# Kernel tuning notes

Measured on AMD Instinct MI355X. Metric: run time of the kernel, lower is better.

The kernel has to match this reference:

```python
import jax, jax.numpy as jnp
import numpy as np

G = 1.0 / 7.0  # grid cell size


def _iou(a, b):
    # a, b: tuples (x1, y1, x2, y2) of broadcastable arrays
    ix1 = jnp.maximum(a[0], b[0])
    iy1 = jnp.maximum(a[1], b[1])
    ix2 = jnp.minimum(a[2], b[2])
    iy2 = jnp.minimum(a[3], b[3])
    inter = jnp.clip(ix2 - ix1, 0.0) * jnp.clip(iy2 - iy1, 0.0)
    area_a = (a[2] - a[0]) * (a[3] - a[1])
    area_b = (b[2] - b[0]) * (b[3] - b[1])
    union = area_a + area_b - inter
    return inter / jnp.where(union == 0.0, 1.0, union)


def setup_inputs() -> dict:
    key = jax.random.key(0)
    k1, k2, k3 = jax.random.split(key, 3)
    B = 8192
    pred = jax.random.uniform(k1, (B, 30, 7, 7), jnp.float32, 0.05, 0.95)
    label = jax.random.uniform(k2, (B, 30, 7, 7), jnp.float32, 0.05, 0.95)
    # channel 4 of label is the objectness indicator, exactly 0 or 1
    obj = (jax.random.uniform(k3, (B, 7, 7)) < 0.3).astype(jnp.float32)
    label = label.at[:, 4].set(obj)
    return {"pred": pred, "label": label}


def _yolo_loss(pred, label, noobj_weight=0.5):
    obj_weight = 1.0 - noobj_weight
    B = pred.shape[0]
    # i indexes axis 2 (paired with x), j indexes axis 3 (paired with y)
    ii = jnp.arange(7, dtype=pred.dtype).reshape(7, 1)
    jj = jnp.arange(7, dtype=pred.dtype).reshape(1, 7)

    def mk_box(x, y, w, h):
        cx = (x + ii) * G
        cy = (y + jj) * G
        return (cx - w / 2, cy - h / 2, cx + w / 2, cy + h / 2)

    b1 = mk_box(pred[:, 0], pred[:, 1], pred[:, 2], pred[:, 3])
    b2 = mk_box(pred[:, 5], pred[:, 6], pred[:, 7], pred[:, 8])
    # label box exactly as in the source (degenerate: x2==x1, y2==y1)
    lx = (label[:, 0] + ii) * G - label[:, 2] / 2
    ly = (label[:, 1] + jj) * G - label[:, 3] / 2
    bl = (lx, ly, lx, ly)

    iou1 = _iou(b1, bl)
    iou2 = _iou(b2, bl)
    sel1 = iou1 > iou2            # (B,7,7): box 1 is responsible
    obj = label[:, 4] == 1.0      # (B,7,7)

    # per-cell coordinate terms for each box
    t1 = (jnp.sum((pred[:, 0:2] - label[:, 0:2]) ** 2, axis=1)
          + jnp.sum((jnp.sqrt(pred[:, 2:4]) - jnp.sqrt(label[:, 2:4])) ** 2, axis=1))
    t2 = (jnp.sum((pred[:, 5:7] - label[:, 5:7]) ** 2, axis=1)
          + jnp.sum((jnp.sqrt(pred[:, 7:9]) - jnp.sqrt(label[:, 7:9])) ** 2, axis=1))
    obj_term = jnp.where(sel1, t1, t2)
    conf_term = jnp.where(sel1, (pred[:, 4] - 1.0) ** 2, (pred[:, 9] - 1.0) ** 2)
    noobj_obj_term = jnp.where(sel1, pred[:, 9] ** 2, pred[:, 4] ** 2)
    noobj_empty_term = pred[:, 4] ** 2 + pred[:, 9] ** 2
    cls_term = jnp.sum((pred[:, 10:] - label[:, 10:]) ** 2, axis=1)

    zero = jnp.zeros((), pred.dtype)
    obj_loss = jnp.sum(jnp.where(obj, obj_term, zero))
    confidence_loss = jnp.sum(jnp.where(obj, conf_term, zero))
    classes_loss = jnp.sum(jnp.where(obj, cls_term, zero))
    noobj_loss = jnp.sum(jnp.where(obj, noobj_obj_term, noobj_empty_term))

    return (obj_loss * obj_weight + noobj_loss * noobj_weight
            + classes_loss + confidence_loss) / B


def reference(pred, label):
    return _yolo_loss(pred, label, noobj_weight=0.5)
```

## Files before the change

kernel.cpp:

```cpp
#include <hip/hip_runtime.h>


__device__ __forceinline__ float sq(float x) { return x * x; }

__global__ __launch_bounds__(256) void yolo_loss_kernel(
    const float* __restrict__ pred, const float* __restrict__ label,
    float* __restrict__ out, int ncells, float inv_B)
{
    const float Gc = 1.0f / 7.0f;
    int g = blockIdx.x * blockDim.x + threadIdx.x;
    float cell = 0.0f;
    if (g < ncells) {
        int b = g / 49;
        int s = g - b * 49;
        int i = s / 7;
        int j = s - i * 7;
        const float* __restrict__ P = pred  + (size_t)b * 1470 + s;
        const float* __restrict__ L = label + (size_t)b * 1470 + s;

        float p[30], l[30];
#pragma unroll
        for (int c = 0; c < 30; ++c) {
            p[c] = P[c * 49];
            l[c] = L[c * 49];
        }

        float fi = (float)i, fj = (float)j;

        float cx1 = (p[0] + fi) * Gc, cy1 = (p[1] + fj) * Gc;
        float a_x1 = cx1 - p[2] * 0.5f, a_y1 = cy1 - p[3] * 0.5f;
        float a_x2 = cx1 + p[2] * 0.5f, a_y2 = cy1 + p[3] * 0.5f;
        float cx2 = (p[5] + fi) * Gc, cy2 = (p[6] + fj) * Gc;
        float b_x1 = cx2 - p[7] * 0.5f, b_y1 = cy2 - p[8] * 0.5f;
        float b_x2 = cx2 + p[7] * 0.5f, b_y2 = cy2 + p[8] * 0.5f;
        float lx = (l[0] + fi) * Gc - l[2] * 0.5f;
        float ly = (l[1] + fj) * Gc - l[3] * 0.5f;

        auto iou_pt = [&](float x1, float y1, float x2, float y2) {
            float ix = fminf(x2, lx) - fmaxf(x1, lx);
            float iy = fminf(y2, ly) - fmaxf(y1, ly);
            float inter = fmaxf(ix, 0.0f) * fmaxf(iy, 0.0f);
            float area_a = (x2 - x1) * (y2 - y1);
            float uni = area_a + 0.0f - inter;
            float denom = (uni == 0.0f) ? 1.0f : uni;
            return inter / denom;
        };

        float iou1 = iou_pt(a_x1, a_y1, a_x2, a_y2);
        float iou2 = iou_pt(b_x1, b_y1, b_x2, b_y2);
        bool sel1 = iou1 > iou2;

        float t1 = sq(p[0] - l[0]) + sq(p[1] - l[1])
                 + sq(sqrtf(p[2]) - sqrtf(l[2])) + sq(sqrtf(p[3]) - sqrtf(l[3]));
        float t2 = sq(p[5] - l[5]) + sq(p[6] - l[6])
                 + sq(sqrtf(p[7]) - sqrtf(l[7])) + sq(sqrtf(p[8]) - sqrtf(l[8]));

        float obj_term     = sel1 ? t1 : t2;
        float conf_term    = sel1 ? sq(p[4] - 1.0f) : sq(p[9] - 1.0f);
        float noobj_obj    = sel1 ? sq(p[9]) : sq(p[4]);
        float noobj_empty  = sq(p[4]) + sq(p[9]);

        float cls = 0.0f;
#pragma unroll
        for (int c = 10; c < 30; ++c) cls += sq(p[c] - l[c]);

        bool obj = (l[4] == 1.0f);
        cell = obj ? (0.5f * obj_term + conf_term + cls + 0.5f * noobj_obj)
                   : (0.5f * noobj_empty);
    }

#pragma unroll
    for (int off = 32; off > 0; off >>= 1)
        cell += __shfl_down(cell, off, 64);

    __shared__ float smem[4];
    int lane = threadIdx.x & 63;
    int wid  = threadIdx.x >> 6;
    if (lane == 0) smem[wid] = cell;
    __syncthreads();
    if (threadIdx.x == 0) {
        float bs = smem[0] + smem[1] + smem[2] + smem[3];
        atomicAdd(out, bs * inv_B);
    }
}

extern "C" void kernel_launch(void* const* d_in, const int* in_sizes, int n_in,
                              void* d_out, int out_size, void* d_ws, size_t ws_size,
                              hipStream_t stream) {
    const float* pred  = (const float*)d_in[0];
    const float* label = (const float*)d_in[1];
    float* out = (float*)d_out;

    int B = in_sizes[0] / (30 * 49);
    int ncells = B * 49;

    hipMemsetAsync(d_out, 0, sizeof(float), stream);

    int block = 256;
    int grid = (ncells + block - 1) / block;
    yolo_loss_kernel<<<grid, block, 0, stream>>>(pred, label, out, ncells,
                                                 1.0f / (float)B);
}
```

Before: 119.9 us.

## Stage per-batch tiles in shared memory with vectorized float4 loads

Each block now copies two whole batch entries of pred and label into LDS using contiguous float4 loads, then computes the 98 cells from LDS. This is meant to replace the strided per-channel scalar global loads with fully coalesced wide loads. In exchange, most threads sit idle during the compute phase, a block barrier separates loading from compute, and the large LDS footprint limits how many blocks fit per CU.

```diff
diff --git a/kernel.cpp b/kernel.cpp
--- a/kernel.cpp
+++ b/kernel.cpp
@@ -1,40 +1,75 @@
 #include <hip/hip_runtime.h>
 
 
+constexpr int WB = 2;
+constexpr int NT = 256;
+constexpr int CH = 30;
+constexpr int SC = 49;
+constexpr int BF = CH * SC;
+
 __device__ __forceinline__ float sq(float x) { return x * x; }
 
-__global__ __launch_bounds__(256) void yolo_loss_kernel(
+__global__ __launch_bounds__(NT) void yolo_loss_kernel(
     const float* __restrict__ pred, const float* __restrict__ label,
-    float* __restrict__ out, int ncells, float inv_B)
+    float* __restrict__ out, int nbatch, float inv_B)
 {
+    __shared__ float sp[WB * BF];
+    __shared__ float sl[WB * BF];
+    __shared__ float swave[NT / 64];
+
+    const int t = threadIdx.x;
+    const int b0 = blockIdx.x * WB;
+    const int nb = min(WB, nbatch - b0);
+    const int nfloat = nb * BF;
+
+    const float* __restrict__ gp = pred  + (size_t)b0 * BF;
+    const float* __restrict__ gl = label + (size_t)b0 * BF;
+
+    if (nfloat == WB * BF) {
+        const float4* __restrict__ p4 = (const float4*)gp;
+        const float4* __restrict__ l4 = (const float4*)gl;
+        float4* sp4 = (float4*)sp;
+        float4* sl4 = (float4*)sl;
+        constexpr int NV = WB * BF / 4;
+        for (int idx = t; idx < NV; idx += NT) {
+            sp4[idx] = p4[idx];
+            sl4[idx] = l4[idx];
+        }
+    } else {
+        for (int idx = t; idx < nfloat; idx += NT) {
+            sp[idx] = gp[idx];
+            sl[idx] = gl[idx];
+        }
+    }
+    __syncthreads();
+
     const float Gc = 1.0f / 7.0f;
-    int g = blockIdx.x * blockDim.x + threadIdx.x;
     float cell = 0.0f;
-    if (g < ncells) {
-        int b = g / 49;
-        int s = g - b * 49;
+    if (t < nb * SC) {
+        int bl = t / SC;
+        int s  = t - bl * SC;
         int i = s / 7;
         int j = s - i * 7;
-        const float* __restrict__ P = pred  + (size_t)b * 1470 + s;
-        const float* __restrict__ L = label + (size_t)b * 1470 + s;
+        const float* __restrict__ p = sp + bl * BF + s;
+        const float* __restrict__ l = sl + bl * BF + s;
 
-        float p[30], l[30];
+        float pv[CH], lv[CH];
 #pragma unroll
-        for (int c = 0; c < 30; ++c) {
-            p[c] = P[c * 49];
-            l[c] = L[c * 49];
+        for (int c = 0; c < CH; ++c) {
+            pv[c] = p[c * SC];
+            lv[c] = l[c * SC];
         }
 
         float fi = (float)i, fj = (float)j;
 
-        float cx1 = (p[0] + fi) * Gc, cy1 = (p[1] + fj) * Gc;
-        float a_x1 = cx1 - p[2] * 0.5f, a_y1 = cy1 - p[3] * 0.5f;
-        float a_x2 = cx1 + p[2] * 0.5f, a_y2 = cy1 + p[3] * 0.5f;
-        float cx2 = (p[5] + fi) * Gc, cy2 = (p[6] + fj) * Gc;
-        float b_x1 = cx2 - p[7] * 0.5f, b_y1 = cy2 - p[8] * 0.5f;
-        float b_x2 = cx2 + p[7] * 0.5f, b_y2 = cy2 + p[8] * 0.5f;
-        float lx = (l[0] + fi) * Gc - l[2] * 0.5f;
-        float ly = (l[1] + fj) * Gc - l[3] * 0.5f;
+        float cx1 = (pv[0] + fi) * Gc, cy1 = (pv[1] + fj) * Gc;
+        float a_x1 = cx1 - pv[2] * 0.5f, a_y1 = cy1 - pv[3] * 0.5f;
+        float a_x2 = cx1 + pv[2] * 0.5f, a_y2 = cy1 + pv[3] * 0.5f;
+        float cx2 = (pv[5] + fi) * Gc, cy2 = (pv[6] + fj) * Gc;
+        float b_x1 = cx2 - pv[7] * 0.5f, b_y1 = cy2 - pv[8] * 0.5f;
+        float b_x2 = cx2 + pv[7] * 0.5f, b_y2 = cy2 + pv[8] * 0.5f;
+        float lx = (lv[0] + fi) * Gc - lv[2] * 0.5f;
+        float ly = (lv[1] + fj) * Gc - lv[3] * 0.5f;
 
         auto iou_pt = [&](float x1, float y1, float x2, float y2) {
             float ix = fminf(x2, lx) - fmaxf(x1, lx);
@@ -50,21 +85,21 @@
         float iou2 = iou_pt(b_x1, b_y1, b_x2, b_y2);
         bool sel1 = iou1 > iou2;
 
-        float t1 = sq(p[0] - l[0]) + sq(p[1] - l[1])
-                 + sq(sqrtf(p[2]) - sqrtf(l[2])) + sq(sqrtf(p[3]) - sqrtf(l[3]));
-        float t2 = sq(p[5] - l[5]) + sq(p[6] - l[6])
-                 + sq(sqrtf(p[7]) - sqrtf(l[7])) + sq(sqrtf(p[8]) - sqrtf(l[8]));
+        float t1 = sq(pv[0] - lv[0]) + sq(pv[1] - lv[1])
+                 + sq(sqrtf(pv[2]) - sqrtf(lv[2])) + sq(sqrtf(pv[3]) - sqrtf(lv[3]));
+        float t2 = sq(pv[5] - lv[5]) + sq(pv[6] - lv[6])
+                 + sq(sqrtf(pv[7]) - sqrtf(lv[7])) + sq(sqrtf(pv[8]) - sqrtf(lv[8]));
 
         float obj_term     = sel1 ? t1 : t2;
-        float conf_term    = sel1 ? sq(p[4] - 1.0f) : sq(p[9] - 1.0f);
-        float noobj_obj    = sel1 ? sq(p[9]) : sq(p[4]);
-        float noobj_empty  = sq(p[4]) + sq(p[9]);
+        float conf_term    = sel1 ? sq(pv[4] - 1.0f) : sq(pv[9] - 1.0f);
+        float noobj_obj    = sel1 ? sq(pv[9]) : sq(pv[4]);
+        float noobj_empty  = sq(pv[4]) + sq(pv[9]);
 
         float cls = 0.0f;
 #pragma unroll
-        for (int c = 10; c < 30; ++c) cls += sq(p[c] - l[c]);
+        for (int c = 10; c < CH; ++c) cls += sq(pv[c] - lv[c]);
 
-        bool obj = (l[4] == 1.0f);
+        bool obj = (lv[4] == 1.0f);
         cell = obj ? (0.5f * obj_term + conf_term + cls + 0.5f * noobj_obj)
                    : (0.5f * noobj_empty);
     }
@@ -73,13 +108,12 @@
     for (int off = 32; off > 0; off >>= 1)
         cell += __shfl_down(cell, off, 64);
 
-    __shared__ float smem[4];
-    int lane = threadIdx.x & 63;
-    int wid  = threadIdx.x >> 6;
-    if (lane == 0) smem[wid] = cell;
+    int lane = t & 63;
+    int wid  = t >> 6;
+    if (lane == 0) swave[wid] = cell;
     __syncthreads();
-    if (threadIdx.x == 0) {
-        float bs = smem[0] + smem[1] + smem[2] + smem[3];
+    if (t == 0) {
+        float bs = swave[0] + swave[1] + swave[2] + swave[3];
         atomicAdd(out, bs * inv_B);
     }
 }
@@ -91,13 +125,11 @@
     const float* label = (const float*)d_in[1];
     float* out = (float*)d_out;
 
-    int B = in_sizes[0] / (30 * 49);
-    int ncells = B * 49;
+    int B = in_sizes[0] / BF;
 
     hipMemsetAsync(d_out, 0, sizeof(float), stream);
 
-    int block = 256;
-    int grid = (ncells + block - 1) / block;
-    yolo_loss_kernel<<<grid, block, 0, stream>>>(pred, label, out, ncells,
-                                                 1.0f / (float)B);
+    int grid = (B + WB - 1) / WB;
+    yolo_loss_kernel<<<grid, NT, 0, stream>>>(pred, label, out, B,
+                                              1.0f / (float)B);
 }
```

Result: slower. 151.4 us (+26.2%).
